# Optimization experiments

Measured on AMD Instinct MI355X. Metric: run time of the kernel, lower is better.

## Reference

```python
import jax, jax.numpy as jnp
import numpy as np

DIM = 768
NUM_HEADS = 12
HEAD_DIM = DIM // NUM_HEADS
SCALE = HEAD_DIM ** -0.5


def setup_inputs() -> dict:
    key = jax.random.key(0)
    ks = jax.random.split(key, 7)
    B, N, C = 8, 1024, DIM
    x = jax.random.normal(ks[0], (B, N, C), dtype=jnp.float32)
    mask = jax.random.randint(ks[1], (B, N), 0, 2) > 0  # True = masked out
    qkv_w = jax.random.normal(ks[2], (3 * C, C), dtype=jnp.float32) * 0.02
    q_bias = jax.random.normal(ks[3], (C,), dtype=jnp.float32) * 0.02
    v_bias = jax.random.normal(ks[4], (C,), dtype=jnp.float32) * 0.02
    proj_w = jax.random.normal(ks[5], (C, C), dtype=jnp.float32) * 0.02
    proj_b = jax.random.normal(ks[6], (C,), dtype=jnp.float32) * 0.02
    return {"x": x, "mask": mask, "qkv_w": qkv_w, "q_bias": q_bias,
            "v_bias": v_bias, "proj_w": proj_w, "proj_b": proj_b}


def reference(x, mask, qkv_w, q_bias, v_bias, proj_w, proj_b):
    B, N, C = x.shape
    # CAE bias: concat(q_bias, zeros, v_bias) for the fused qkv projection
    qkv_bias = jnp.concatenate([q_bias, jnp.zeros_like(v_bias), v_bias])
    qkv = x @ qkv_w.T + qkv_bias  # [B, N, 3C]
    qkv = qkv.reshape(B, N, 3, NUM_HEADS, HEAD_DIM)
    q, k, v = (qkv[:, :, i].transpose(0, 2, 1, 3) for i in range(3))  # [B,H,N,hd]
    attn = jnp.einsum('bhqd,bhkd->bhqk', q * SCALE, k)  # [B,H,N,N]
    attn = jnp.where(mask[:, None, None, :], -jnp.inf, attn)
    attn = jax.nn.softmax(attn, axis=-1)
    out = jnp.einsum('bhqk,bhkd->bhqd', attn, v)  # [B,H,N,hd]
    out = out.transpose(0, 2, 1, 3).reshape(B, N, C)
    return out @ proj_w.T + proj_b
```

## Files before the change

### kernel.cpp

```cpp
#include <hip/hip_runtime.h>
#include <cstddef>
#include <cstdint>


typedef __attribute__((ext_vector_type(4))) float f32x4;
typedef __attribute__((ext_vector_type(8))) __bf16 bf16x8;
typedef __attribute__((ext_vector_type(4))) unsigned int uint4v;
typedef __attribute__((ext_vector_type(2))) unsigned int uint2v;

#define QK_PRESCALE 0.18033688011112042f

__device__ __forceinline__ unsigned short f2bf(float f) {
  return (unsigned short)((__float_as_uint(f) + 0x8000u) >> 16);
}
__device__ __forceinline__ unsigned int pack2bf(float flo, float fhi) {
  unsigned ulo = __float_as_uint(flo) + 0x8000u;
  unsigned uhi = __float_as_uint(fhi) + 0x8000u;
  return __builtin_amdgcn_perm(uhi, ulo, 0x07060302);
}

__device__ __forceinline__ void gl_lds16(const unsigned short* g, unsigned short* l) {
  __builtin_amdgcn_global_load_lds(
      (const __attribute__((address_space(1))) unsigned int*)g,
      (__attribute__((address_space(3))) unsigned int*)l, 16, 0, 0);
}

__global__ __launch_bounds__(256)
void cvt3_kernel(const float* __restrict__ s0, unsigned short* __restrict__ d0,
                 const float* __restrict__ s1, unsigned short* __restrict__ d1,
                 const float* __restrict__ s2, unsigned short* __restrict__ d2,
                 const int* __restrict__ mask, int* __restrict__ idxA,
                 int* __restrict__ nkA) {
  __shared__ int sc[256];
  int bid = blockIdx.x;
  if (bid >= 8448) {
    const int b = bid - 8448;
    const int t = threadIdx.x;
    int4 mv = ((const int4*)(mask + b * 1024))[t];
    int c = (mv.x == 0) + (mv.y == 0) + (mv.z == 0) + (mv.w == 0);
    sc[t] = c;
    __syncthreads();
    for (int off = 1; off < 256; off <<= 1) {
      int v = (t >= off) ? sc[t - off] : 0;
      __syncthreads();
      sc[t] += v;
      __syncthreads();
    }
    int run = sc[t] - c;
#pragma unroll
    for (int i = 0; i < 4; ++i) {
      int tok = t * 4 + i;
      int m = (i == 0) ? mv.x : (i == 1) ? mv.y : (i == 2) ? mv.z : mv.w;
      if (!m) { idxA[b * 1024 + run] = tok; run++; }
    }
    if (t == 0) nkA[b] = sc[255];
    return;
  }
  const float* s; unsigned short* d; int i; int n4;
  if (bid < 6144)      { s = s0; d = d0; i = bid * 256 + threadIdx.x;            n4 = 1572864; }
  else if (bid < 7872) { s = s1; d = d1; i = (bid - 6144) * 256 + threadIdx.x;   n4 = 442368; }
  else                 { s = s2; d = d2; i = (bid - 7872) * 256 + threadIdx.x;   n4 = 147456; }
  if (i < n4) {
    float4 v = ((const float4*)s)[i];
    uint2v o;
    o.x = pack2bf(v.x, v.y);
    o.y = pack2bf(v.z, v.w);
    ((uint2v*)d)[i] = o;
  }
}

__global__ __launch_bounds__(256, 3)
void qkv_gemm(const unsigned short* __restrict__ xb, const unsigned short* __restrict__ wb,
              const float* __restrict__ qb, const float* __restrict__ vb,
              unsigned short* __restrict__ qo, unsigned short* __restrict__ ko,
              unsigned short* __restrict__ vto) {
  __shared__ __align__(16) unsigned short lds[20480];
  const int tid = threadIdx.x;
  const int lane = tid & 63, wid = tid >> 6;
  const int widu = __builtin_amdgcn_readfirstlane(wid);
  const int lm = lane & 15, lq = lane >> 4;
  const int xsw = lm & 7;
  const int wr = widu >> 1, wc = widu & 1;
  const int L = blockIdx.x;
  const int xcd = L & 7, s = L >> 3;
  const int ft = s >> 3;
  const int tt = xcd * 8 + (s & 7);
  const int m0 = tt * 128;
  const int n0 = ft * 192;
  const int srow = lane >> 3;
  const int scolsw = ((lane & 7) ^ srow) * 8;
  const unsigned short* paS = wb + (size_t)(n0 + widu * 48 + srow) * 768 + scolsw;
  const unsigned short* pbS = xb + (size_t)(m0 + widu * 32 + srow) * 768 + scolsw;
  unsigned short* const ldsA = &lds[(widu * 48) * 64];
  unsigned short* const ldsB = &lds[12288 + (widu * 32) * 64];

  f32x4 acc[6][4] = {};

  for (int t = 0; t < 12; ++t) {
    const size_t c = (size_t)t * 64;
#pragma unroll
    for (int i = 0; i < 6; ++i)
      gl_lds16(paS + (size_t)i * 8 * 768 + c, ldsA + i * 8 * 64);
#pragma unroll
    for (int i = 0; i < 4; ++i)
      gl_lds16(pbS + (size_t)i * 8 * 768 + c, ldsB + i * 8 * 64);
    __syncthreads();

    bf16x8 bff[4][2], af[3][2];
#pragma unroll
    for (int n2 = 0; n2 < 4; ++n2)
#pragma unroll
      for (int kx = 0; kx < 2; ++kx)
        bff[n2][kx] = *(const bf16x8*)&lds[12288 + (wc * 64 + n2 * 16 + lm) * 64 + (((kx * 4 + lq) ^ xsw) * 8)];
#pragma unroll
    for (int m2 = 0; m2 < 3; ++m2)
#pragma unroll
      for (int kx = 0; kx < 2; ++kx)
        af[m2][kx] = *(const bf16x8*)&lds[(wr * 96 + m2 * 16 + lm) * 64 + (((kx * 4 + lq) ^ xsw) * 8)];

    __builtin_amdgcn_s_setprio(1);
#pragma unroll
    for (int kx = 0; kx < 2; ++kx)
#pragma unroll
      for (int m2 = 0; m2 < 3; ++m2)
#pragma unroll
        for (int n2 = 0; n2 < 4; ++n2)
          acc[m2][n2] = __builtin_amdgcn_mfma_f32_16x16x32_bf16(af[m2][kx], bff[n2][kx], acc[m2][n2], 0, 0, 0);
    __builtin_amdgcn_s_setprio(0);

    bf16x8 af2[3][2];
#pragma unroll
    for (int m2 = 0; m2 < 3; ++m2)
#pragma unroll
      for (int kx = 0; kx < 2; ++kx)
        af2[m2][kx] = *(const bf16x8*)&lds[(wr * 96 + (3 + m2) * 16 + lm) * 64 + (((kx * 4 + lq) ^ xsw) * 8)];
    __builtin_amdgcn_s_setprio(1);
#pragma unroll
    for (int kx = 0; kx < 2; ++kx)
#pragma unroll
      for (int m2 = 0; m2 < 3; ++m2)
#pragma unroll
        for (int n2 = 0; n2 < 4; ++n2)
          acc[3 + m2][n2] = __builtin_amdgcn_mfma_f32_16x16x32_bf16(af2[m2][kx], bff[n2][kx], acc[3 + m2][n2], 0, 0, 0);
    __builtin_amdgcn_s_setprio(0);

    __syncthreads();
  }

  const int bq = tt >> 3;
  const int tokb = (tt & 7) * 128;
  if (n0 < 1536) {
    const bool isq = n0 < 768;
    unsigned short* dst0 = isq ? qo : ko;
#pragma unroll
    for (int mi = 0; mi < 6; ++mi) {
      const int fblk = n0 + wr * 96 + mi * 16;
      const int fd = fblk - (isq ? 0 : 768);
      const int hh = fd >> 6;
      const int dih = (fd & 63) + lq * 4;
      f32x4 bias4 = {0.f, 0.f, 0.f, 0.f};
      if (isq) bias4 = *(const f32x4*)&qb[fblk + lq * 4];
#pragma unroll
      for (int ni = 0; ni < 4; ++ni) {
        const int tok = tokb + wc * 64 + ni * 16 + lm;
        uint2v pk;
        if (isq) {
          pk.x = pack2bf((acc[mi][ni][0] + bias4[0]) * QK_PRESCALE,
                         (acc[mi][ni][1] + bias4[1]) * QK_PRESCALE);
          pk.y = pack2bf((acc[mi][ni][2] + bias4[2]) * QK_PRESCALE,
                         (acc[mi][ni][3] + bias4[3]) * QK_PRESCALE);
        } else {
          pk.x = pack2bf(acc[mi][ni][0], acc[mi][ni][1]);
          pk.y = pack2bf(acc[mi][ni][2], acc[mi][ni][3]);
        }
        *(uint2v*)&dst0[(((size_t)(bq * 12 + hh)) * 1024 + tok) * 64 + dih] = pk;
      }
    }
  } else {
    const int vb0 = n0 - 1536;
#pragma unroll
    for (int p = 0; p < 2; ++p) {
      __syncthreads();
      if (wr == p) {
#pragma unroll
        for (int mi = 0; mi < 6; ++mi) {
          f32x4 bias4 = *(const f32x4*)&vb[vb0 + p * 96 + mi * 16 + lq * 4];
#pragma unroll
          for (int ni = 0; ni < 4; ++ni) {
            const int tokl = wc * 64 + ni * 16 + lm;
#pragma unroll
            for (int r = 0; r < 4; ++r)
              lds[(mi * 16 + lq * 4 + r) * 136 + tokl] = f2bf(acc[mi][ni][r] + bias4[r]);
          }
        }
      }
      __syncthreads();
      for (int r = tid >> 1; r < 96; r += 128) {
        const int tq = tid & 1;
        const int dgv = vb0 + p * 96 + r;
        const int hh = dgv >> 6, d = dgv & 63;
        unsigned short* dstv = vto + (((size_t)(bq * 12 + hh)) * 64 + d) * 1024 + tokb + tq * 64;
        const unsigned short* srcr = &lds[r * 136 + tq * 64];
#pragma unroll
        for (int j = 0; j < 8; ++j)
          *(uint4v*)&dstv[j * 8] = *(const uint4v*)&srcr[j * 8];
      }
    }
  }
}

__global__ __launch_bounds__(1024)
void gather_kv(const unsigned short* __restrict__ ko, const unsigned short* __restrict__ vto,
               const int* __restrict__ idxA, const int* __restrict__ nkA,
               unsigned short* __restrict__ kc, unsigned short* __restrict__ vtc) {
  __shared__ int idxL[1024];
  const int bh = blockIdx.x;
  const int b = bh / 12;
  const int t = threadIdx.x;
  const int nk = nkA[b];
  if (t < 256)
    ((int4*)idxL)[t] = ((const int4*)(idxA + b * 1024))[t];
  __syncthreads();
  const int w = t >> 6, lane = t & 63;
  const unsigned short* kin = ko + (size_t)bh * 65536;
  unsigned short* kout = kc + (size_t)bh * 65536;
  for (int j = w; j < 1024; j += 16) {
    int src = idxL[j] & 1023;
    unsigned short v = kin[(size_t)src * 64 + lane];
    kout[(size_t)j * 64 + lane] = (j < nk) ? v : (unsigned short)0;
  }
  const unsigned short* vin = vto + (size_t)bh * 65536;
  unsigned short* vout = vtc + (size_t)bh * 65536;
  for (int d = w; d < 64; d += 16) {
    const unsigned short* vr = vin + (size_t)d * 1024;
    unsigned short* vo = vout + (size_t)d * 1024;
    for (int c0 = 0; c0 < 1024; c0 += 64) {
      int j = c0 + lane;
      int src = idxL[j] & 1023;
      unsigned short v = vr[src];
      vo[j] = (j < nk) ? v : (unsigned short)0;
    }
  }
}

__global__ __launch_bounds__(256, 4)
void attn_mfma(const unsigned short* __restrict__ q, const unsigned short* __restrict__ kcp,
               const unsigned short* __restrict__ vtc, const int* __restrict__ nkA,
               unsigned short* __restrict__ ao) {
  __shared__ unsigned short ks_s[2][64 * 64];
  __shared__ unsigned short vs_s[2][64 * 64];
  __shared__ float mkl[1024];
  const int tid = threadIdx.x;
  const int lane = tid & 63, wid = tid >> 6;
  const int lm = lane & 15, lq = lane >> 4;
  const int xsw = lm & 7;
  const int plq = ((lq & 1) << 1) | (lq >> 1);
  const int L = blockIdx.x;
  const int xcd = L & 7, s = L >> 3;
  const int bh = xcd * 12 + s / 8;
  const int qt = s % 8;
  const int bb = bh / 12, hh = bh % 12;
  const unsigned short* qp = q + (size_t)bh * 65536;
  const unsigned short* kp = kcp + (size_t)bh * 65536;
  const unsigned short* vp = vtc + (size_t)bh * 65536;
  const int nk = nkA[bb];
  int nkt = (nk + 63) >> 6;
  if (nkt < 1) nkt = 1;
  const int q0 = qt * 128 + wid * 32;
  const int srow = lane >> 3;
  const int scolsw = ((lane & 7) ^ srow) * 8;
  const unsigned short* gk = kp + (size_t)(wid * 16 + srow) * 64 + scolsw;
  const unsigned short* gv = vp + (size_t)(wid * 16 + srow) * 1024 + scolsw;

#define STAGE_T(kt_, b_) { \
    gl_lds16(gk + (size_t)(kt_) * 4096, &ks_s[b_][(wid * 16) * 64]); \
    gl_lds16(gk + (size_t)(kt_) * 4096 + (size_t)8 * 64, &ks_s[b_][(wid * 16 + 8) * 64]); \
    gl_lds16(gv + (size_t)(kt_) * 64, &vs_s[b_][(wid * 16) * 64]); \
    gl_lds16(gv + (size_t)(kt_) * 64 + (size_t)8 * 1024, &vs_s[b_][(wid * 16 + 8) * 64]); }

  {
    int j4 = tid * 4;
    float4 f;
    f.x = (j4 + 0 < nk) ? 0.0f : -1e30f;
    f.y = (j4 + 1 < nk) ? 0.0f : -1e30f;
    f.z = (j4 + 2 < nk) ? 0.0f : -1e30f;
    f.w = (j4 + 3 < nk) ? 0.0f : -1e30f;
    ((float4*)mkl)[tid] = f;
  }

  bf16x8 qf[2][2];
#pragma unroll
  for (int mi = 0; mi < 2; ++mi)
#pragma unroll
    for (int ks2 = 0; ks2 < 2; ++ks2)
      qf[mi][ks2] = *(const bf16x8*)&qp[(size_t)(q0 + mi * 16 + lm) * 64 + ks2 * 32 + lq * 8];
  bf16x8 ones;
#pragma unroll
  for (int i = 0; i < 8; ++i) ones[i] = (__bf16)1.0f;

  f32x4 o_acc[2][4] = {};
  f32x4 l_acc[2] = {};

  STAGE_T(0, 0);
  __syncthreads();

  for (int kt = 0; kt < nkt; ++kt) {
    const int b = kt & 1;
    if (kt) {
      asm volatile("s_waitcnt vmcnt(0)\ns_barrier" ::: "memory");
    }
    if (kt + 1 < nkt) STAGE_T(kt + 1, b ^ 1);

    f32x4 st[4][2] = {};
#pragma unroll
    for (int ks2 = 0; ks2 < 2; ++ks2) {
      bf16x8 kf[4];
#pragma unroll
      for (int nt = 0; nt < 4; ++nt)
        kf[nt] = *(const bf16x8*)&ks_s[b][(nt * 16 + lm) * 64 + (((ks2 * 4 + lq) ^ xsw) * 8)];
      __builtin_amdgcn_s_setprio(1);
#pragma unroll
      for (int nt = 0; nt < 4; ++nt)
#pragma unroll
        for (int mi = 0; mi < 2; ++mi)
          st[nt][mi] = __builtin_amdgcn_mfma_f32_16x16x32_bf16(kf[nt], qf[mi][ks2], st[nt][mi], 0, 0, 0);
      __builtin_amdgcn_s_setprio(0);
    }

#pragma unroll
    for (int h2 = 0; h2 < 2; ++h2) {
      bf16x8 pf[2];
#pragma unroll
      for (int mi = 0; mi < 2; ++mi) {
        const int ntA = h2 * 2, ntB = h2 * 2 + 1;
        f32x4 mvA = *(const f32x4*)&mkl[kt * 64 + ntA * 16 + lq * 4];
        f32x4 mvB = *(const f32x4*)&mkl[kt * 64 + ntB * 16 + lq * 4];
        unsigned a0 = pack2bf(__builtin_amdgcn_exp2f(st[ntA][mi][0] + mvA[0]),
                              __builtin_amdgcn_exp2f(st[ntA][mi][1] + mvA[1]));
        unsigned a1 = pack2bf(__builtin_amdgcn_exp2f(st[ntA][mi][2] + mvA[2]),
                              __builtin_amdgcn_exp2f(st[ntA][mi][3] + mvA[3]));
        unsigned b0 = pack2bf(__builtin_amdgcn_exp2f(st[ntB][mi][0] + mvB[0]),
                              __builtin_amdgcn_exp2f(st[ntB][mi][1] + mvB[1]));
        unsigned b1 = pack2bf(__builtin_amdgcn_exp2f(st[ntB][mi][2] + mvB[2]),
                              __builtin_amdgcn_exp2f(st[ntB][mi][3] + mvB[3]));
        asm volatile("v_permlane16_swap_b32 %0, %1" : "+v"(a0), "+v"(b0));
        asm volatile("v_permlane16_swap_b32 %0, %1" : "+v"(a1), "+v"(b1));
        uint4v u; u.x = a0; u.y = a1; u.z = b0; u.w = b1;
        pf[mi] = __builtin_bit_cast(bf16x8, u);
      }
      bf16x8 vf[4];
#pragma unroll
      for (int nt = 0; nt < 4; ++nt)
        vf[nt] = *(const bf16x8*)&vs_s[b][(nt * 16 + lm) * 64 + (((h2 * 4 + plq) ^ xsw) * 8)];
      __builtin_amdgcn_s_setprio(1);
#pragma unroll
      for (int mi = 0; mi < 2; ++mi) {
#pragma unroll
        for (int nt = 0; nt < 4; ++nt)
          o_acc[mi][nt] = __builtin_amdgcn_mfma_f32_16x16x32_bf16(pf[mi], vf[nt], o_acc[mi][nt], 0, 0, 0);
        l_acc[mi] = __builtin_amdgcn_mfma_f32_16x16x32_bf16(pf[mi], ones, l_acc[mi], 0, 0, 0);
      }
      __builtin_amdgcn_s_setprio(0);
    }
  }
#undef STAGE_T

#pragma unroll
  for (int mi = 0; mi < 2; ++mi) {
#pragma unroll
    for (int r = 0; r < 4; ++r) {
      float inv = 1.0f / l_acc[mi][r];
      int tok = q0 + mi * 16 + lq * 4 + r;
#pragma unroll
      for (int nt = 0; nt < 4; ++nt)
        ao[(size_t)(bb * 1024 + tok) * 768 + hh * 64 + nt * 16 + lm] = f2bf(o_acc[mi][nt][r] * inv);
    }
  }
}

__global__ __launch_bounds__(256, 2)
void proj_gemm(const unsigned short* __restrict__ ab, const unsigned short* __restrict__ wb,
               const float* __restrict__ pb, float* __restrict__ out) {
  __shared__ __align__(16) unsigned short lds[14336];
  const int tid = threadIdx.x;
  const int lane = tid & 63, wid = tid >> 6;
  const int widu = __builtin_amdgcn_readfirstlane(wid);
  const int lm = lane & 15, lq = lane >> 4;
  const int xsw = lm & 7;
  const int wr = widu >> 1, wc = widu & 1;
  const int L = blockIdx.x;
  const int xcd = L & 7, s = L >> 3;
  const int n0 = (s >> 3) * 96;
  const int m0 = (xcd * 8 + (s & 7)) * 128;
  const int srow = lane >> 3;
  const int scolsw = ((lane & 7) ^ srow) * 8;
  const unsigned short* paS = wb + (size_t)(n0 + widu * 24 + srow) * 768 + scolsw;
  const unsigned short* pbS = ab + (size_t)(m0 + widu * 32 + srow) * 768 + scolsw;
  unsigned short* const ldsA = &lds[(widu * 24) * 64];
  unsigned short* const ldsB = &lds[6144 + (widu * 32) * 64];

  f32x4 acc[3][4] = {};

  for (int t = 0; t < 12; ++t) {
    const size_t c = (size_t)t * 64;
#pragma unroll
    for (int i = 0; i < 3; ++i)
      gl_lds16(paS + (size_t)i * 8 * 768 + c, ldsA + i * 8 * 64);
#pragma unroll
    for (int i = 0; i < 4; ++i)
      gl_lds16(pbS + (size_t)i * 8 * 768 + c, ldsB + i * 8 * 64);
    __syncthreads();

    bf16x8 af[3][2], bff[4][2];
#pragma unroll
    for (int m2 = 0; m2 < 3; ++m2)
#pragma unroll
      for (int kx = 0; kx < 2; ++kx)
        af[m2][kx] = *(const bf16x8*)&lds[(wr * 48 + m2 * 16 + lm) * 64 + (((kx * 4 + lq) ^ xsw) * 8)];
#pragma unroll
    for (int n2 = 0; n2 < 4; ++n2)
#pragma unroll
      for (int kx = 0; kx < 2; ++kx)
        bff[n2][kx] = *(const bf16x8*)&lds[6144 + (wc * 64 + n2 * 16 + lm) * 64 + (((kx * 4 + lq) ^ xsw) * 8)];

    __builtin_amdgcn_s_setprio(1);
#pragma unroll
    for (int kx = 0; kx < 2; ++kx)
#pragma unroll
      for (int m2 = 0; m2 < 3; ++m2)
#pragma unroll
        for (int n2 = 0; n2 < 4; ++n2)
          acc[m2][n2] = __builtin_amdgcn_mfma_f32_16x16x32_bf16(af[m2][kx], bff[n2][kx], acc[m2][n2], 0, 0, 0);
    __builtin_amdgcn_s_setprio(0);

    __syncthreads();
  }

#pragma unroll
  for (int mi = 0; mi < 3; ++mi) {
    int gn0 = n0 + wr * 48 + mi * 16 + lq * 4;
    f32x4 bias4 = *(const f32x4*)&pb[gn0];
#pragma unroll
    for (int ni = 0; ni < 4; ++ni) {
      int gm = m0 + wc * 64 + ni * 16 + lm;
      f32x4 o;
      o[0] = acc[mi][ni][0] + bias4[0];
      o[1] = acc[mi][ni][1] + bias4[1];
      o[2] = acc[mi][ni][2] + bias4[2];
      o[3] = acc[mi][ni][3] + bias4[3];
      *(f32x4*)&out[(size_t)gm * 768 + gn0] = o;
    }
  }
}

extern "C" void kernel_launch(void* const* d_in, const int* in_sizes, int n_in,
                              void* d_out, int out_size, void* d_ws, size_t ws_size,
                              hipStream_t stream) {
  const float* x      = (const float*)d_in[0];
  const int*   mask   = (const int*)d_in[1];
  const float* qkv_w  = (const float*)d_in[2];
  const float* q_bias = (const float*)d_in[3];
  const float* v_bias = (const float*)d_in[4];
  const float* proj_w = (const float*)d_in[5];
  const float* proj_b = (const float*)d_in[6];
  float* out = (float*)d_out;
  unsigned short* p = (unsigned short*)d_ws;
  unsigned short* xb     = p;              p += 6291456;
  unsigned short* wqkvb  = p;              p += 1769472;
  unsigned short* wprojb = p;              p += 589824;
  unsigned short* qo     = p;              p += 6291456;
  unsigned short* ko     = p;              p += 6291456;
  unsigned short* vto    = p;              p += 6291456;
  unsigned short* ao     = p;              p += 6291456;
  unsigned short* kc     = p;              p += 6291456;
  unsigned short* vtc    = p;              p += 6291456;
  int* idxA = (int*)p;
  int* nkA  = idxA + 8192;

  cvt3_kernel<<<8456, 256, 0, stream>>>(x, xb, qkv_w, wqkvb, proj_w, wprojb,
                                        mask, idxA, nkA);
  qkv_gemm<<<768, 256, 0, stream>>>(xb, wqkvb, q_bias, v_bias, qo, ko, vto);
  gather_kv<<<96, 1024, 0, stream>>>(ko, vto, idxA, nkA, kc, vtc);
  attn_mfma<<<768, 256, 0, stream>>>(qo, kc, vtc, nkA, ao);
  proj_gemm<<<512, 256, 0, stream>>>(ao, wprojb, proj_b, out);
}
```

Measured before the change: 179.8 us.

## Fuse K/V compaction into QKV GEMM epilogue via scattered stores

Drops the separate gather_kv kernel. The mask prefix scan now writes per-token destination positions (posA) instead of a compacted index list, and the QKV GEMM epilogue scatters K rows and V-transposed elements straight into the compacted kc/vtc buffers, skipping masked tokens. The cvt kernel zero-fills the padding region up to the next multiple of 64. This removes a full read and write of K and V plus one launch. The cost is that V stores become scalar 2-byte scattered writes in place of 16-byte vector stores, and the padding fill is a serial per-batch loop.

```diff
diff --git a/kernel.cpp b/kernel.cpp
--- a/kernel.cpp
+++ b/kernel.cpp
@@ -29,8 +29,9 @@
 void cvt3_kernel(const float* __restrict__ s0, unsigned short* __restrict__ d0,
                  const float* __restrict__ s1, unsigned short* __restrict__ d1,
                  const float* __restrict__ s2, unsigned short* __restrict__ d2,
-                 const int* __restrict__ mask, int* __restrict__ idxA,
-                 int* __restrict__ nkA) {
+                 const int* __restrict__ mask, int* __restrict__ posA,
+                 int* __restrict__ nkA,
+                 unsigned short* __restrict__ kc, unsigned short* __restrict__ vtc) {
   __shared__ int sc[256];
   int bid = blockIdx.x;
   if (bid >= 8448) {
@@ -47,13 +48,26 @@
       __syncthreads();
     }
     int run = sc[t] - c;
+    const int nk = sc[255];
 #pragma unroll
     for (int i = 0; i < 4; ++i) {
       int tok = t * 4 + i;
       int m = (i == 0) ? mv.x : (i == 1) ? mv.y : (i == 2) ? mv.z : mv.w;
-      if (!m) { idxA[b * 1024 + run] = tok; run++; }
-    }
-    if (t == 0) nkA[b] = sc[255];
+      posA[b * 1024 + tok] = run;
+      if (!m) run++;
+    }
+    if (t == 0) nkA[b] = nk;
+    int nk64 = (nk + 63) & ~63;
+    if (nk64 < 64) nk64 = 64;
+    const int pad = nk64 - nk;
+    for (int h = 0; h < 12; ++h) {
+      size_t base = (size_t)(b * 12 + h) * 65536;
+      for (int i = t; i < pad * 64; i += 256)
+        kc[base + (size_t)nk * 64 + i] = 0;
+      for (int d = 0; d < 64; ++d)
+        for (int i = t; i < pad; i += 256)
+          vtc[base + (size_t)d * 1024 + nk + i] = 0;
+    }
     return;
   }
   const float* s; unsigned short* d; int i; int n4;
@@ -72,9 +86,12 @@
 __global__ __launch_bounds__(256, 3)
 void qkv_gemm(const unsigned short* __restrict__ xb, const unsigned short* __restrict__ wb,
               const float* __restrict__ qb, const float* __restrict__ vb,
-              unsigned short* __restrict__ qo, unsigned short* __restrict__ ko,
-              unsigned short* __restrict__ vto) {
+              const int* __restrict__ mask, const int* __restrict__ posA,
+              unsigned short* __restrict__ qo, unsigned short* __restrict__ kc,
+              unsigned short* __restrict__ vtc) {
   __shared__ __align__(16) unsigned short lds[20480];
+  __shared__ int posL2[128];
+  __shared__ int vldL2[128];
   const int tid = threadIdx.x;
   const int lane = tid & 63, wid = tid >> 6;
   const int widu = __builtin_amdgcn_readfirstlane(wid);
@@ -149,35 +166,56 @@
 
   const int bq = tt >> 3;
   const int tokb = (tt & 7) * 128;
-  if (n0 < 1536) {
-    const bool isq = n0 < 768;
-    unsigned short* dst0 = isq ? qo : ko;
+  if (n0 < 768) {
 #pragma unroll
     for (int mi = 0; mi < 6; ++mi) {
       const int fblk = n0 + wr * 96 + mi * 16;
-      const int fd = fblk - (isq ? 0 : 768);
-      const int hh = fd >> 6;
-      const int dih = (fd & 63) + lq * 4;
-      f32x4 bias4 = {0.f, 0.f, 0.f, 0.f};
-      if (isq) bias4 = *(const f32x4*)&qb[fblk + lq * 4];
+      const int hh = fblk >> 6;
+      const int dih = (fblk & 63) + lq * 4;
+      f32x4 bias4 = *(const f32x4*)&qb[fblk + lq * 4];
 #pragma unroll
       for (int ni = 0; ni < 4; ++ni) {
         const int tok = tokb + wc * 64 + ni * 16 + lm;
         uint2v pk;
-        if (isq) {
-          pk.x = pack2bf((acc[mi][ni][0] + bias4[0]) * QK_PRESCALE,
-                         (acc[mi][ni][1] + bias4[1]) * QK_PRESCALE);
-          pk.y = pack2bf((acc[mi][ni][2] + bias4[2]) * QK_PRESCALE,
-                         (acc[mi][ni][3] + bias4[3]) * QK_PRESCALE);
-        } else {
-          pk.x = pack2bf(acc[mi][ni][0], acc[mi][ni][1]);
-          pk.y = pack2bf(acc[mi][ni][2], acc[mi][ni][3]);
-        }
-        *(uint2v*)&dst0[(((size_t)(bq * 12 + hh)) * 1024 + tok) * 64 + dih] = pk;
+        pk.x = pack2bf((acc[mi][ni][0] + bias4[0]) * QK_PRESCALE,
+                       (acc[mi][ni][1] + bias4[1]) * QK_PRESCALE);
+        pk.y = pack2bf((acc[mi][ni][2] + bias4[2]) * QK_PRESCALE,
+                       (acc[mi][ni][3] + bias4[3]) * QK_PRESCALE);
+        *(uint2v*)&qo[(((size_t)(bq * 12 + hh)) * 1024 + tok) * 64 + dih] = pk;
+      }
+    }
+  } else if (n0 < 1536) {
+    const int* pmk = mask + bq * 1024;
+    const int* pps = posA + bq * 1024;
+    int pv[4], vv[4];
+#pragma unroll
+    for (int ni = 0; ni < 4; ++ni) {
+      const int tok = tokb + wc * 64 + ni * 16 + lm;
+      vv[ni] = (pmk[tok] == 0);
+      pv[ni] = pps[tok];
+    }
+#pragma unroll
+    for (int mi = 0; mi < 6; ++mi) {
+      const int fblk = n0 + wr * 96 + mi * 16;
+      const int fd = fblk - 768;
+      const int hh = fd >> 6;
+      const int dih = (fd & 63) + lq * 4;
+#pragma unroll
+      for (int ni = 0; ni < 4; ++ni) {
+        uint2v pk;
+        pk.x = pack2bf(acc[mi][ni][0], acc[mi][ni][1]);
+        pk.y = pack2bf(acc[mi][ni][2], acc[mi][ni][3]);
+        if (vv[ni])
+          *(uint2v*)&kc[(((size_t)(bq * 12 + hh)) * 1024 + pv[ni]) * 64 + dih] = pk;
       }
     }
   } else {
     const int vb0 = n0 - 1536;
+    for (int i = tid; i < 128; i += 256) {
+      const int tok = tokb + i;
+      posL2[i] = posA[bq * 1024 + tok];
+      vldL2[i] = (mask[bq * 1024 + tok] == 0);
+    }
 #pragma unroll
     for (int p = 0; p < 2; ++p) {
       __syncthreads();
@@ -199,46 +237,14 @@
         const int tq = tid & 1;
         const int dgv = vb0 + p * 96 + r;
         const int hh = dgv >> 6, d = dgv & 63;
-        unsigned short* dstv = vto + (((size_t)(bq * 12 + hh)) * 64 + d) * 1024 + tokb + tq * 64;
+        const size_t base = (((size_t)(bq * 12 + hh)) * 64 + d) * 1024;
         const unsigned short* srcr = &lds[r * 136 + tq * 64];
-#pragma unroll
-        for (int j = 0; j < 8; ++j)
-          *(uint4v*)&dstv[j * 8] = *(const uint4v*)&srcr[j * 8];
-      }
-    }
-  }
-}
-
-__global__ __launch_bounds__(1024)
-void gather_kv(const unsigned short* __restrict__ ko, const unsigned short* __restrict__ vto,
-               const int* __restrict__ idxA, const int* __restrict__ nkA,
-               unsigned short* __restrict__ kc, unsigned short* __restrict__ vtc) {
-  __shared__ int idxL[1024];
-  const int bh = blockIdx.x;
-  const int b = bh / 12;
-  const int t = threadIdx.x;
-  const int nk = nkA[b];
-  if (t < 256)
-    ((int4*)idxL)[t] = ((const int4*)(idxA + b * 1024))[t];
-  __syncthreads();
-  const int w = t >> 6, lane = t & 63;
-  const unsigned short* kin = ko + (size_t)bh * 65536;
-  unsigned short* kout = kc + (size_t)bh * 65536;
-  for (int j = w; j < 1024; j += 16) {
-    int src = idxL[j] & 1023;
-    unsigned short v = kin[(size_t)src * 64 + lane];
-    kout[(size_t)j * 64 + lane] = (j < nk) ? v : (unsigned short)0;
-  }
-  const unsigned short* vin = vto + (size_t)bh * 65536;
-  unsigned short* vout = vtc + (size_t)bh * 65536;
-  for (int d = w; d < 64; d += 16) {
-    const unsigned short* vr = vin + (size_t)d * 1024;
-    unsigned short* vo = vout + (size_t)d * 1024;
-    for (int c0 = 0; c0 < 1024; c0 += 64) {
-      int j = c0 + lane;
-      int src = idxL[j] & 1023;
-      unsigned short v = vr[src];
-      vo[j] = (j < nk) ? v : (unsigned short)0;
+#pragma unroll 8
+        for (int j = 0; j < 64; ++j) {
+          const int ii = tq * 64 + j;
+          if (vldL2[ii]) vtc[base + posL2[ii]] = srcr[j];
+        }
+      }
     }
   }
 }
@@ -469,18 +475,15 @@
   unsigned short* wqkvb  = p;              p += 1769472;
   unsigned short* wprojb = p;              p += 589824;
   unsigned short* qo     = p;              p += 6291456;
-  unsigned short* ko     = p;              p += 6291456;
-  unsigned short* vto    = p;              p += 6291456;
-  unsigned short* ao     = p;              p += 6291456;
   unsigned short* kc     = p;              p += 6291456;
   unsigned short* vtc    = p;              p += 6291456;
-  int* idxA = (int*)p;
-  int* nkA  = idxA + 8192;
+  unsigned short* ao     = p;              p += 6291456;
+  int* posA = (int*)p;
+  int* nkA  = posA + 8192;
 
   cvt3_kernel<<<8456, 256, 0, stream>>>(x, xb, qkv_w, wqkvb, proj_w, wprojb,
-                                        mask, idxA, nkA);
-  qkv_gemm<<<768, 256, 0, stream>>>(xb, wqkvb, q_bias, v_bias, qo, ko, vto);
-  gather_kv<<<96, 1024, 0, stream>>>(ko, vto, idxA, nkA, kc, vtc);
+                                        mask, posA, nkA, kc, vtc);
+  qkv_gemm<<<768, 256, 0, stream>>>(xb, wqkvb, q_bias, v_bias, mask, posA, qo, kc, vtc);
   attn_mfma<<<768, 256, 0, stream>>>(qo, kc, vtc, nkA, ao);
   proj_gemm<<<512, 256, 0, stream>>>(ao, wprojb, proj_b, out);
 }
```

New measurement: 242.9 us. +35.1%, slower.
